# Kernel optimization log

Measured on AMD Instinct MI355X. Metric: run time of the kernel, lower is better.

The kernel has to match this reference:

```python
import jax, jax.numpy as jnp
import numpy as np

N = 200000
MUL = 64
# e3nn normalization (irrep_normalization='component', path_normalization='element'):
# FCTP(irreps, '1x0e', irreps): per-out-irrep norm sqrt(dim)/sqrt(num_elements) * w3j(l,0,l)=1/sqrt(dim)
#   -> overall 1/sqrt(mul_in)
INV_SQRT_MUL = 1.0 / np.sqrt(MUL)        # lin0 / sc : single path, fan-in 64
INV_SQRT_2MUL = 1.0 / np.sqrt(2 * MUL)   # final lin : two mid paths feed each output irrep (fan-in 128)
INV_SQRT3 = 1.0 / np.sqrt(3.0)           # w3j(1,1,0) dot-product CG coefficient


def setup_inputs() -> dict:
    key = jax.random.key(0)
    ks = jax.random.split(key, 12)
    f = lambda k, s: jax.random.normal(k, s, dtype=jnp.float32)
    return {
        'x1': f(ks[0], (N, 4 * MUL)),          # node feats: 64x0e + 64x1o
        'edge_attr': f(ks[1], (N, 4)),         # 1x0e + 1x1o spherical harmonics
        'tp_weight': f(ks[2], (N, 4 * MUL)),   # external uvu weights, 4 paths x 64
        'node_attr': f(ks[3], (N, 1)),         # 1x0e scalar attrs
        'W_lin0_s': f(ks[4], (MUL, MUL)),
        'W_lin0_v': f(ks[5], (MUL, MUL)),
        'W_sc_s': f(ks[6], (MUL, MUL)),
        'W_sc_v': f(ks[7], (MUL, MUL)),
        'W_lin_A': f(ks[8], (MUL, MUL)),
        'W_lin_D': f(ks[9], (MUL, MUL)),
        'W_lin_B': f(ks[10], (MUL, MUL)),
        'W_lin_C': f(ks[11], (MUL, MUL)),
    }


def _fctp_scalar_attr(s, v, a, Ws, Wv, c):
    # FullyConnectedTensorProduct(mul x {0e,1o}, 1x0e, mul x {0e,1o}) with scalar attr a: [N,1]
    out_s = c * a * (s @ Ws)                                   # [N,64]
    out_v = c * a[:, :, None] * jnp.einsum('num,uw->nwm', v, Wv)  # [N,64,3]
    return out_s, out_v


def reference(x1, edge_attr, tp_weight, node_attr,
              W_lin0_s, W_lin0_v, W_sc_s, W_sc_v,
              W_lin_A, W_lin_D, W_lin_B, W_lin_C):
    n = x1.shape[0]
    s = x1[:, :MUL]                     # 64x0e
    v = x1[:, MUL:].reshape(n, MUL, 3)  # 64x1o
    a = node_attr                       # [N,1]
    e0 = edge_attr[:, :1]               # 1x0e
    e1 = edge_attr[:, 1:4]              # 1x1o

    # self-connection and input linear (both FCTP with scalar node attrs)
    sc_s, sc_v = _fctp_scalar_attr(s, v, a, W_sc_s, W_sc_v, INV_SQRT_MUL)
    s0, v0 = _fctp_scalar_attr(s, v, a, W_lin0_s, W_lin0_v, INV_SQRT_MUL)

    # uvu TensorProduct with external per-element weights; instruction order A,B,C,D
    wA = tp_weight[:, 0:MUL]
    wB = tp_weight[:, MUL:2 * MUL]
    wC = tp_weight[:, 2 * MUL:3 * MUL]
    wD = tp_weight[:, 3 * MUL:4 * MUL]
    midA = wA * s0 * e0                                              # 0e x 0e -> 0e
    midB = wB[:, :, None] * s0[:, :, None] * e1[:, None, :]         # 0e x 1o -> 1o
    midC = wC[:, :, None] * v0 * e0[:, :, None]                     # 1o x 0e -> 1o
    midD = INV_SQRT3 * wD * jnp.einsum('num,nm->nu', v0, e1)        # 1o x 1o -> 0e (dot)
    # dropout (e3nn irrep dropout) in eval mode == identity

    # final FCTP(irreps_mid, 1x0e, irreps_out): two mid paths per output irrep
    out_s = INV_SQRT_2MUL * a * (midA @ W_lin_A + midD @ W_lin_D)
    out_v = INV_SQRT_2MUL * a[:, :, None] * (
        jnp.einsum('num,uw->nwm', midB, W_lin_B)
        + jnp.einsum('num,uw->nwm', midC, W_lin_C))

    out_s = out_s + sc_s
    out_v = out_v + sc_v
    return jnp.concatenate([out_s, out_v.reshape(n, 3 * MUL)], axis=1)
```

## Files before the change

### kernel.cpp

```cpp
#include <hip/hip_runtime.h>

typedef __attribute__((ext_vector_type(4))) float f32x4;
typedef __attribute__((ext_vector_type(8))) short bf16x8;

#define MFMA(a, b, c) __builtin_amdgcn_mfma_f32_16x16x32_bf16(a, b, c, 0, 0, 0)
#define NOPS asm volatile("s_nop 7\ns_nop 7\ns_nop 7\ns_nop 7" ::: "memory")

static __device__ __forceinline__ void split2(float x, short& hi, short& lo) {
  union { float f; unsigned u; } v; v.f = x;
  unsigned uh = v.u & 0xFFFF0000u;
  hi = (short)(uh >> 16);
  union { unsigned u; float f; } w; w.u = uh;
  union { float f; unsigned u; } z; z.f = x - w.f;
  lo = (short)((z.u + 0x7FFFu + ((z.u >> 16) & 1u)) >> 16);
}

__global__ void prep_w(const float* __restrict__ W0, const float* __restrict__ W1,
                       const float* __restrict__ W2, const float* __restrict__ W3,
                       const float* __restrict__ W4, const float* __restrict__ W5,
                       const float* __restrict__ W6, const float* __restrict__ W7,
                       short* __restrict__ ws) {
  const float* W[8] = {W0, W1, W2, W3, W4, W5, W6, W7};
  int t = blockIdx.x * 256 + threadIdx.x;
  int lane = t & 63, fragid = (t >> 6) & 7, mat = t >> 9;
  const float* Wm = W[mat];
  int ct = fragid >> 1, kh = fragid & 1;
  int wcol = ct * 16 + (lane & 15);
  int k0 = kh * 32 + ((lane >> 4) << 3);
  bf16x8 vh, vl;
#pragma unroll
  for (int j = 0; j < 8; ++j) {
    short h, l;
    split2(Wm[(k0 + j) * 64 + wcol], h, l);
    vh[j] = h; vl[j] = l;
  }
  size_t base = ((size_t)(mat * 16) + fragid) * 512 + lane * 8;
  *(bf16x8*)(ws + base) = vh;
  *(bf16x8*)(ws + base + 4096) = vl;
}

struct BF { bf16x8 h[4][2], l[4][2]; };

static __device__ __forceinline__ void loadB(const short* __restrict__ ws, int mat, int lane,
                                             BF& B) {
#pragma unroll
  for (int ct = 0; ct < 4; ++ct)
#pragma unroll
    for (int kh = 0; kh < 2; ++kh) {
      B.h[ct][kh] = *(const bf16x8*)(ws + ((size_t)(mat * 16) + ct * 2 + kh) * 512 + lane * 8);
      B.l[ct][kh] = *(const bf16x8*)(ws + ((size_t)(mat * 16 + 8) + ct * 2 + kh) * 512 + lane * 8);
    }
}

static __device__ __forceinline__ void cluster(const bf16x8 (&ah)[2], const bf16x8 (&al)[2],
                                               const BF& B, f32x4 (&acc)[4]) {
  __builtin_amdgcn_sched_barrier(0);
#pragma unroll
  for (int ct = 0; ct < 4; ++ct)
#pragma unroll
    for (int kh = 0; kh < 2; ++kh) {
      acc[ct] = MFMA(ah[kh], B.h[ct][kh], acc[ct]);
      acc[ct] = MFMA(al[kh], B.h[ct][kh], acc[ct]);
      acc[ct] = MFMA(ah[kh], B.l[ct][kh], acc[ct]);
    }
  __builtin_amdgcn_sched_barrier(0);
  NOPS;
}

static __device__ __forceinline__ void ldpair(const short* lds_s, int plane_hi, int arow, int lane,
                                              bf16x8 (&ah)[2], bf16x8 (&al)[2]) {
#pragma unroll
  for (int kh = 0; kh < 2; ++kh) {
    int off = arow * 72 + kh * 32 + ((lane >> 4) << 3);
    ah[kh] = *(const bf16x8*)(lds_s + plane_hi * 4608 + off);
    al[kh] = *(const bf16x8*)(lds_s + (plane_hi + 1) * 4608 + off);
  }
}

__global__ __launch_bounds__(256, 2) void fused_tp(
    const float* __restrict__ x1, const float* __restrict__ edge,
    const float* __restrict__ tp, const float* __restrict__ node,
    const short* __restrict__ ws, float* __restrict__ out) {
  __shared__ short lds_s[8 * 4608];
  __shared__ float cst[64 * 6];
  const int t = threadIdx.x;
  const int R0 = blockIdx.x * 64;

  {
    int c = t;
    int plane_hi, u;
    if (c < 64) { plane_hi = 0; u = c; }
    else { int q = c - 64; u = q / 3; int m = q - u * 3; plane_hi = 2 + 2 * m; }
    short* phi = lds_s + plane_hi * 4608 + u;
    short* plo = phi + 4608;
    const float* xc = x1 + (size_t)R0 * 256 + c;
#pragma unroll 8
    for (int i = 0; i < 64; ++i) {
      short h, l;
      split2(xc[(size_t)i * 256], h, l);
      phi[i * 72] = h; plo[i * 72] = l;
    }
    if (t < 64) {
      f32x4 e = *(const f32x4*)(edge + (size_t)(R0 + t) * 4);
      float a = node[R0 + t];
      float* cr = cst + t * 6;
      cr[0] = e[0]; cr[1] = e[1]; cr[2] = e[2]; cr[3] = e[3];
      cr[4] = 0.125f * 0.08838834764831845f * a * a;
      cr[5] = 0.125f * a;
    }
  }
  __syncthreads();

  const int lane = t & 63;
  const int wid = t >> 6;
  const int r0 = wid * 16;
  const int lg = lane >> 4;
  const int arow = r0 + (lane & 15);
  const f32x4 z = {0.f, 0.f, 0.f, 0.f};

  f32x4 scs[4], s0v[4], scv[3][4], v0v[3][4];
#pragma unroll
  for (int ct = 0; ct < 4; ++ct) { scs[ct] = z; s0v[ct] = z; }
#pragma unroll
  for (int m = 0; m < 3; ++m)
#pragma unroll
    for (int ct = 0; ct < 4; ++ct) { scv[m][ct] = z; v0v[m][ct] = z; }
  {
    BF B;
    bf16x8 ah[2], al[2];
    ldpair(lds_s, 0, arow, lane, ah, al);
    loadB(ws, 0, lane, B); cluster(ah, al, B, scs);
    loadB(ws, 1, lane, B); cluster(ah, al, B, s0v);
    loadB(ws, 2, lane, B);
#pragma unroll
    for (int m = 0; m < 3; ++m) {
      ldpair(lds_s, 2 + 2 * m, arow, lane, ah, al);
      cluster(ah, al, B, scv[m]);
    }
    loadB(ws, 3, lane, B);
#pragma unroll
    for (int m = 0; m < 3; ++m) {
      ldpair(lds_s, 2 + 2 * m, arow, lane, ah, al);
      cluster(ah, al, B, v0v[m]);
    }
  }
  __syncthreads();

#pragma unroll
  for (int reg = 0; reg < 4; ++reg) {
    int n = r0 + (lg << 2) + reg;
    const float* cr = cst + n * 6;
    float e0 = cr[0], e1x = cr[1], e1y = cr[2], e1z = cr[3];
    const float* tr = tp + (size_t)(R0 + n) * 256;
#pragma unroll
    for (int ct = 0; ct < 4; ++ct) {
      int w = ct * 16 + (lane & 15);
      float s0 = s0v[ct][reg];
      float dot = v0v[0][ct][reg] * e1x + v0v[1][ct][reg] * e1y + v0v[2][ct][reg] * e1z;
      int off = n * 72 + w;
      short h, l;
      split2(tr[w] * s0 * e0, h, l);      lds_s[off] = h;            lds_s[4608 + off] = l;
      split2(tr[64 + w] * s0, h, l);      lds_s[2 * 4608 + off] = h; lds_s[3 * 4608 + off] = l;
      split2(tr[192 + w] * dot * 0.5773502691896258f, h, l);
                                          lds_s[4 * 4608 + off] = h; lds_s[5 * 4608 + off] = l;
    }
  }
  __syncthreads();

  f32x4 gAD[4], gB[4];
#pragma unroll
  for (int ct = 0; ct < 4; ++ct) { gAD[ct] = z; gB[ct] = z; }
  {
    BF B;
    bf16x8 ah[2], al[2];
    loadB(ws, 4, lane, B);
    ldpair(lds_s, 0, arow, lane, ah, al);
    cluster(ah, al, B, gAD);
    loadB(ws, 5, lane, B);
    ldpair(lds_s, 4, arow, lane, ah, al);
    cluster(ah, al, B, gAD);
    loadB(ws, 6, lane, B);
    ldpair(lds_s, 2, arow, lane, ah, al);
    cluster(ah, al, B, gB);
  }

#pragma unroll
  for (int reg = 0; reg < 4; ++reg) {
    int n = r0 + (lg << 2) + reg;
    const float* cr = cst + n * 6;
    float kp = cr[4], ksc = cr[5];
    float* orow = out + (size_t)(R0 + n) * 256;
#pragma unroll
    for (int ct = 0; ct < 4; ++ct) {
      int w = ct * 16 + (lane & 15);
      orow[w] = kp * gAD[ct][reg] + ksc * scs[ct][reg];
    }
  }
  __syncthreads();

#pragma unroll
  for (int reg = 0; reg < 4; ++reg) {
    int n = r0 + (lg << 2) + reg;
    float e0 = cst[n * 6];
    const float* tr = tp + (size_t)(R0 + n) * 256;
#pragma unroll
    for (int ct = 0; ct < 4; ++ct) {
      int w = ct * 16 + (lane & 15);
      float wc = tr[128 + w];
      int off = n * 72 + w;
#pragma unroll
      for (int m = 0; m < 3; ++m) {
        short h, l;
        split2(wc * v0v[m][ct][reg] * e0, h, l);
        lds_s[(2 * m) * 4608 + off] = h;
        lds_s[(2 * m + 1) * 4608 + off] = l;
      }
    }
  }
  __syncthreads();

  f32x4 gC[3][4];
#pragma unroll
  for (int m = 0; m < 3; ++m)
#pragma unroll
    for (int ct = 0; ct < 4; ++ct) gC[m][ct] = z;
  {
    BF B;
    loadB(ws, 7, lane, B);
#pragma unroll
    for (int m = 0; m < 3; ++m) {
      bf16x8 ah[2], al[2];
      ldpair(lds_s, 2 * m, arow, lane, ah, al);
      cluster(ah, al, B, gC[m]);
    }
  }

#pragma unroll
  for (int reg = 0; reg < 4; ++reg) {
    int n = r0 + (lg << 2) + reg;
    const float* cr = cst + n * 6;
    float e1x = cr[1], e1y = cr[2], e1z = cr[3], kp = cr[4], ksc = cr[5];
    float* orow = out + (size_t)(R0 + n) * 256;
#pragma unroll
    for (int ct = 0; ct < 4; ++ct) {
      int w = ct * 16 + (lane & 15);
      float vx = kp * (e1x * gB[ct][reg] + gC[0][ct][reg]) + ksc * scv[0][ct][reg];
      float vy = kp * (e1y * gB[ct][reg] + gC[1][ct][reg]) + ksc * scv[1][ct][reg];
      float vz = kp * (e1z * gB[ct][reg] + gC[2][ct][reg]) + ksc * scv[2][ct][reg];
      float* vp = orow + 64 + 3 * w;
      vp[0] = vx; vp[1] = vy; vp[2] = vz;
    }
  }
}

extern "C" void kernel_launch(void* const* d_in, const int* in_sizes, int n_in,
                              void* d_out, int out_size, void* d_ws, size_t ws_size,
                              hipStream_t stream) {
  const float* x1   = (const float*)d_in[0];
  const float* edge = (const float*)d_in[1];
  const float* tp   = (const float*)d_in[2];
  const float* node = (const float*)d_in[3];
  short* ws = (short*)d_ws;
  int n = in_sizes[0] / 256;

  prep_w<<<16, 256, 0, stream>>>(
      (const float*)d_in[6], (const float*)d_in[4],
      (const float*)d_in[7], (const float*)d_in[5],
      (const float*)d_in[8], (const float*)d_in[9],
      (const float*)d_in[10], (const float*)d_in[11], ws);

  fused_tp<<<n / 64, 256, 0, stream>>>(x1, edge, tp, node, ws, (float*)d_out);
}
```

Before: 180.8 us.

## Swizzle LDS planes, double-buffer weight fragments, and round-to-nearest bf16 split

Replaces the padded LDS layout (row stride 72 shorts) with an unpadded 128-byte row layout using an XOR swizzle, shrinking LDS from 8x4608 to 8x4096 shorts. It also keeps two B-fragment register sets so weight loads are issued ahead of the MFMA clusters, and merges the scv and v0v loops so each A fragment is loaded once and used for both. The hi part of the bf16 split now uses round-to-nearest instead of truncation. The aim is fewer LDS bank conflicts, fewer LDS reads and better hiding of weight-load latency, at the cost of extra registers that may pressure occupancy at two blocks per CU.

Result: slower. 373.9 us (+106.8%).

```diff
diff --git a/kernel.cpp b/kernel.cpp
--- a/kernel.cpp
+++ b/kernel.cpp
@@ -6,13 +6,17 @@
 #define MFMA(a, b, c) __builtin_amdgcn_mfma_f32_16x16x32_bf16(a, b, c, 0, 0, 0)
 #define NOPS asm volatile("s_nop 7\ns_nop 7\ns_nop 7\ns_nop 7" ::: "memory")
 
+static __device__ __forceinline__ short rnebf(float x) {
+  union { float f; unsigned u; } v; v.f = x;
+  return (short)((v.u + 0x7FFFu + ((v.u >> 16) & 1u)) >> 16);
+}
+static __device__ __forceinline__ float bf2f(short h) {
+  union { unsigned u; float f; } v; v.u = ((unsigned)(unsigned short)h) << 16;
+  return v.f;
+}
 static __device__ __forceinline__ void split2(float x, short& hi, short& lo) {
-  union { float f; unsigned u; } v; v.f = x;
-  unsigned uh = v.u & 0xFFFF0000u;
-  hi = (short)(uh >> 16);
-  union { unsigned u; float f; } w; w.u = uh;
-  union { float f; unsigned u; } z; z.f = x - w.f;
-  lo = (short)((z.u + 0x7FFFu + ((z.u >> 16) & 1u)) >> 16);
+  hi = rnebf(x);
+  lo = rnebf(x - bf2f(hi));
 }
 
 __global__ void prep_w(const float* __restrict__ W0, const float* __restrict__ W1,
@@ -67,21 +71,29 @@
   NOPS;
 }
 
-static __device__ __forceinline__ void ldpair(const short* lds_s, int plane_hi, int arow, int lane,
-                                              bf16x8 (&ah)[2], bf16x8 (&al)[2]) {
+static __device__ __forceinline__ void ldM(const short* __restrict__ M, int ph, int arow,
+                                           int lane, bf16x8 (&ah)[2], bf16x8 (&al)[2]) {
+  int swz = (arow & 7) << 4;
 #pragma unroll
   for (int kh = 0; kh < 2; ++kh) {
-    int off = arow * 72 + kh * 32 + ((lane >> 4) << 3);
-    ah[kh] = *(const bf16x8*)(lds_s + plane_hi * 4608 + off);
-    al[kh] = *(const bf16x8*)(lds_s + (plane_hi + 1) * 4608 + off);
-  }
+    int ab = (arow * 128 + kh * 64 + ((lane >> 4) << 4)) ^ swz;
+    ah[kh] = *(const bf16x8*)((const char*)M + ph * 8192 + ab);
+    al[kh] = *(const bf16x8*)((const char*)M + (ph + 1) * 8192 + ab);
+  }
+}
+static __device__ __forceinline__ void stM(short* __restrict__ M, int p, int n, int w, float x) {
+  short h, l;
+  split2(x, h, l);
+  int ab = (n * 128 + w * 2) ^ ((n & 7) << 4);
+  *(short*)((char*)M + p * 8192 + ab) = h;
+  *(short*)((char*)M + (p + 1) * 8192 + ab) = l;
 }
 
 __global__ __launch_bounds__(256, 2) void fused_tp(
     const float* __restrict__ x1, const float* __restrict__ edge,
     const float* __restrict__ tp, const float* __restrict__ node,
     const short* __restrict__ ws, float* __restrict__ out) {
-  __shared__ short lds_s[8 * 4608];
+  __shared__ short lds_s[8 * 4096];
   __shared__ float cst[64 * 6];
   const int t = threadIdx.x;
   const int R0 = blockIdx.x * 64;
@@ -91,14 +103,16 @@
     int plane_hi, u;
     if (c < 64) { plane_hi = 0; u = c; }
     else { int q = c - 64; u = q / 3; int m = q - u * 3; plane_hi = 2 + 2 * m; }
-    short* phi = lds_s + plane_hi * 4608 + u;
-    short* plo = phi + 4608;
+    char* phi = (char*)lds_s + plane_hi * 8192;
+    char* plo = phi + 8192;
     const float* xc = x1 + (size_t)R0 * 256 + c;
 #pragma unroll 8
     for (int i = 0; i < 64; ++i) {
       short h, l;
       split2(xc[(size_t)i * 256], h, l);
-      phi[i * 72] = h; plo[i * 72] = l;
+      int ab = (i * 128 + u * 2) ^ ((i & 7) << 4);
+      *(short*)(phi + ab) = h;
+      *(short*)(plo + ab) = l;
     }
     if (t < 64) {
       f32x4 e = *(const f32x4*)(edge + (size_t)(R0 + t) * 4);
@@ -126,22 +140,20 @@
 #pragma unroll
     for (int ct = 0; ct < 4; ++ct) { scv[m][ct] = z; v0v[m][ct] = z; }
   {
-    BF B;
+    BF B0, B1;
     bf16x8 ah[2], al[2];
-    ldpair(lds_s, 0, arow, lane, ah, al);
-    loadB(ws, 0, lane, B); cluster(ah, al, B, scs);
-    loadB(ws, 1, lane, B); cluster(ah, al, B, s0v);
-    loadB(ws, 2, lane, B);
+    loadB(ws, 0, lane, B0);
+    loadB(ws, 1, lane, B1);
+    ldM(lds_s, 0, arow, lane, ah, al);
+    cluster(ah, al, B0, scs);
+    loadB(ws, 2, lane, B0);
+    cluster(ah, al, B1, s0v);
+    loadB(ws, 3, lane, B1);
 #pragma unroll
     for (int m = 0; m < 3; ++m) {
-      ldpair(lds_s, 2 + 2 * m, arow, lane, ah, al);
-      cluster(ah, al, B, scv[m]);
-    }
-    loadB(ws, 3, lane, B);
-#pragma unroll
-    for (int m = 0; m < 3; ++m) {
-      ldpair(lds_s, 2 + 2 * m, arow, lane, ah, al);
-      cluster(ah, al, B, v0v[m]);
+      ldM(lds_s, 2 + 2 * m, arow, lane, ah, al);
+      cluster(ah, al, B0, scv[m]);
+      cluster(ah, al, B1, v0v[m]);
     }
   }
   __syncthreads();
@@ -157,12 +169,9 @@
       int w = ct * 16 + (lane & 15);
       float s0 = s0v[ct][reg];
       float dot = v0v[0][ct][reg] * e1x + v0v[1][ct][reg] * e1y + v0v[2][ct][reg] * e1z;
-      int off = n * 72 + w;
-      short h, l;
-      split2(tr[w] * s0 * e0, h, l);      lds_s[off] = h;            lds_s[4608 + off] = l;
-      split2(tr[64 + w] * s0, h, l);      lds_s[2 * 4608 + off] = h; lds_s[3 * 4608 + off] = l;
-      split2(tr[192 + w] * dot * 0.5773502691896258f, h, l);
-                                          lds_s[4 * 4608 + off] = h; lds_s[5 * 4608 + off] = l;
+      stM(lds_s, 0, n, w, tr[w] * s0 * e0);
+      stM(lds_s, 2, n, w, tr[64 + w] * s0);
+      stM(lds_s, 4, n, w, tr[192 + w] * dot * 0.5773502691896258f);
     }
   }
   __syncthreads();
@@ -171,17 +180,17 @@
 #pragma unroll
   for (int ct = 0; ct < 4; ++ct) { gAD[ct] = z; gB[ct] = z; }
   {
-    BF B;
+    BF B0, B1;
     bf16x8 ah[2], al[2];
-    loadB(ws, 4, lane, B);
-    ldpair(lds_s, 0, arow, lane, ah, al);
-    cluster(ah, al, B, gAD);
-    loadB(ws, 5, lane, B);
-    ldpair(lds_s, 4, arow, lane, ah, al);
-    cluster(ah, al, B, gAD);
-    loadB(ws, 6, lane, B);
-    ldpair(lds_s, 2, arow, lane, ah, al);
-    cluster(ah, al, B, gB);
+    loadB(ws, 4, lane, B0);
+    loadB(ws, 5, lane, B1);
+    ldM(lds_s, 0, arow, lane, ah, al);
+    cluster(ah, al, B0, gAD);
+    loadB(ws, 6, lane, B0);
+    ldM(lds_s, 4, arow, lane, ah, al);
+    cluster(ah, al, B1, gAD);
+    ldM(lds_s, 2, arow, lane, ah, al);
+    cluster(ah, al, B0, gB);
   }
 
 #pragma unroll
@@ -207,14 +216,8 @@
     for (int ct = 0; ct < 4; ++ct) {
       int w = ct * 16 + (lane & 15);
       float wc = tr[128 + w];
-      int off = n * 72 + w;
-#pragma unroll
-      for (int m = 0; m < 3; ++m) {
-        short h, l;
-        split2(wc * v0v[m][ct][reg] * e0, h, l);
-        lds_s[(2 * m) * 4608 + off] = h;
-        lds_s[(2 * m + 1) * 4608 + off] = l;
-      }
+#pragma unroll
+      for (int m = 0; m < 3; ++m) stM(lds_s, 2 * m, n, w, wc * v0v[m][ct][reg] * e0);
     }
   }
   __syncthreads();
@@ -225,13 +228,13 @@
 #pragma unroll
     for (int ct = 0; ct < 4; ++ct) gC[m][ct] = z;
   {
-    BF B;
-    loadB(ws, 7, lane, B);
+    BF B0;
+    loadB(ws, 7, lane, B0);
 #pragma unroll
     for (int m = 0; m < 3; ++m) {
       bf16x8 ah[2], al[2];
-      ldpair(lds_s, 2 * m, arow, lane, ah, al);
-      cluster(ah, al, B, gC[m]);
+      ldM(lds_s, 2 * m, arow, lane, ah, al);
+      cluster(ah, al, B0, gC[m]);
     }
   }
 
```
